# Performance work log

Hardware: AMD Instinct MI355X
Metric: run time of the kernel (lower is better)

The kernel has to match this reference:

```python
import jax, jax.numpy as jnp
import numpy as np

N_NODES = 100000
N_EDGES = 1600000
IN_F = 256
OUT_F = 128


def setup_inputs() -> dict:
    key = jax.random.key(0)
    ks = jax.random.split(key, 6)
    stdv = 1.0 / np.sqrt(OUT_F)
    x = jax.random.normal(ks[0], (N_NODES, IN_F), dtype=jnp.float32)
    edge_row = jax.random.randint(ks[1], (N_EDGES,), 0, N_NODES)
    edge_col = jax.random.randint(ks[2], (N_EDGES,), 0, N_NODES)
    edge_val = jax.random.uniform(ks[3], (N_EDGES,), dtype=jnp.float32)
    weight = jax.random.uniform(ks[4], (IN_F, OUT_F), minval=-stdv, maxval=stdv, dtype=jnp.float32)
    bias = jax.random.uniform(ks[5], (OUT_F,), minval=-stdv, maxval=stdv, dtype=jnp.float32)
    return {"x": x, "edge_row": edge_row, "edge_col": edge_col,
            "edge_val": edge_val, "weight": weight, "bias": bias}


def reference(x, edge_row, edge_col, edge_val, weight, bias):
    # support = input @ W                       [N, out]
    support = x @ weight
    # output = spmm(adj, support): for each edge (r, c, v),
    # out[r] += v * support[c]  -- gather then segment-sum over destinations.
    gathered = support[edge_col] * edge_val[:, None]   # [E, out]
    out = jax.ops.segment_sum(gathered, edge_row, num_segments=N_NODES)
    return out + bias
```

## Files before the change

### kernel.cpp

```cpp
#include <hip/hip_runtime.h>
#include <hip/hip_bf16.h>

#define N_NODES 100000
#define N_EDGES 1600000
#define IN_F 256
#define OUT_F 128

#define NBUCK 782
#define CH 4096
#define NCHB ((N_EDGES + CH - 1) / CH)
#define HCAP 2048
#define BCAP 3072

typedef __attribute__((ext_vector_type(8))) short bhalf8;
typedef __attribute__((ext_vector_type(4))) float f32x4;

static __device__ __forceinline__ unsigned short f2bfs(float f) {
    __hip_bfloat16 h = __float2bfloat16(f);
    return *reinterpret_cast<unsigned short*>(&h);
}

__global__ __launch_bounds__(256) void wt_kernel(
    const float* __restrict__ W, unsigned short* __restrict__ Wt)
{
    const int idx = blockIdx.x * 256 + threadIdx.x;
    const int col = idx >> 8;
    const int k   = idx & 255;
    Wt[idx] = f2bfs(W[(size_t)k * OUT_F + col]);
}

__global__ __launch_bounds__(512) void gemm_mfma_kernel(
    const float* __restrict__ x, const unsigned short* __restrict__ Wt,
    unsigned short* __restrict__ support)
{
    __shared__ unsigned short Bs[128 * 256];

    const int tid = threadIdx.x;

    {
        const int row = tid >> 2;
        const int q   = tid & 3;
        const uint4* src = (const uint4*)(Wt + (size_t)row * 256);
        uint4* dst       = (uint4*)(Bs + (size_t)row * 256);
        const int sw = row & 7;
        #pragma unroll
        for (int i = q * 8; i < q * 8 + 8; ++i)
            dst[i ^ sw] = src[i];
    }
    __syncthreads();

    const int wave = tid >> 6, lane = tid & 63;
    const int r_lo = lane & 15;
    const int kq   = lane >> 4;
    const int row0 = blockIdx.x * 128 + wave * 16;

    const float* xa = x + (size_t)min(row0 + r_lo, N_NODES - 1) * IN_F + kq * 8;

    f32x4 acc[8];
    #pragma unroll
    for (int c = 0; c < 8; ++c) acc[c] = (f32x4)0.f;

    #pragma unroll
    for (int ks = 0; ks < 8; ++ks) {
        const float4 al = *(const float4*)(xa + ks * 32);
        const float4 ah = *(const float4*)(xa + ks * 32 + 4);

        bhalf8 A;
        A[0] = (short)f2bfs(al.x); A[1] = (short)f2bfs(al.y);
        A[2] = (short)f2bfs(al.z); A[3] = (short)f2bfs(al.w);
        A[4] = (short)f2bfs(ah.x); A[5] = (short)f2bfs(ah.y);
        A[6] = (short)f2bfs(ah.z); A[7] = (short)f2bfs(ah.w);

        #pragma unroll
        for (int cf = 0; cf < 8; ++cf) {
            const int col = cf * 16 + r_lo;
            const int off = ((ks * 32 + kq * 8) ^ ((col & 7) << 3));
            const bhalf8 B = *(const bhalf8*)(Bs + (size_t)col * 256 + off);
            acc[cf] = __builtin_amdgcn_mfma_f32_16x16x32_bf16(A, B, acc[cf], 0, 0, 0);
        }
    }

    #pragma unroll
    for (int r = 0; r < 4; ++r) {
        const int row = row0 + kq * 4 + r;
        if (row < N_NODES) {
            unsigned short* dst = support + (size_t)row * OUT_F + r_lo;
            #pragma unroll
            for (int cf = 0; cf < 8; ++cf)
                dst[cf * 16] = f2bfs(acc[cf][r]);
        }
    }
}

__global__ __launch_bounds__(512) void bscatter_kernel(
    const int* __restrict__ erow, const int* __restrict__ ecol,
    const float* __restrict__ eval, int* __restrict__ bcnt,
    int2* __restrict__ ebuf)
{
    __shared__ int h[NBUCK];
    __shared__ int cur[NBUCK];
    __shared__ int gbase[NBUCK];
    __shared__ int ps[512];
    __shared__ unsigned short bb[CH];
    __shared__ int2 buf[CH];

    const int tid = threadIdx.x;
    const int e0  = blockIdx.x * CH;
    const int e1  = min(e0 + CH, N_EDGES);
    const int n   = e1 - e0;

    for (int i = tid; i < NBUCK; i += 512) h[i] = 0;
    __syncthreads();

    for (int e = e0 + tid; e < e1; e += 512)
        atomicAdd(&h[erow[e] >> 7], 1);
    __syncthreads();

    {
        const int idx0 = tid * 2;
        int sum = 0;
        #pragma unroll
        for (int k = 0; k < 2; ++k) { const int ii = idx0 + k; if (ii < NBUCK) sum += h[ii]; }
        ps[tid] = sum;
        __syncthreads();
        for (int off = 1; off < 512; off <<= 1) {
            const int a  = (tid >= off) ? ps[tid - off] : 0;
            const int x0 = ps[tid];
            __syncthreads();
            ps[tid] = x0 + a;
            __syncthreads();
        }
        int run = (tid == 0) ? 0 : ps[tid - 1];
        #pragma unroll
        for (int k = 0; k < 2; ++k) {
            const int ii = idx0 + k;
            if (ii < NBUCK) { cur[ii] = run; run += h[ii]; }
        }
    }
    __syncthreads();

    for (int e = e0 + tid; e < e1; e += 512) {
        const int r = erow[e];
        const int b = r >> 7;
        const int p = atomicAdd(&cur[b], 1);
        buf[p] = make_int2(((r & 127) << 17) | ecol[e], __float_as_int(eval[e]));
        bb[p]  = (unsigned short)b;
    }
    __syncthreads();

    for (int i = tid; i < NBUCK; i += 512)
        gbase[i] = h[i] ? (i * BCAP + atomicAdd(&bcnt[i], h[i])) : 0;
    __syncthreads();

    for (int i = tid; i < n; i += 512) {
        const int b  = bb[i];
        const int lb = cur[b] - h[b];
        ebuf[gbase[b] + (i - lb)] = buf[i];
    }
}

__global__ __launch_bounds__(256) void hspmm_kernel(
    const int* __restrict__ bcnt, const int2* __restrict__ ebuf,
    const unsigned short* __restrict__ support,
    const float* __restrict__ bias, float* __restrict__ out)
{
    __shared__ int2 srt[HCAP];
    __shared__ int rc[64];
    __shared__ int rb[65];
    __shared__ int cc[64];

    const int blk = blockIdx.x;
    const int pb  = blk >> 1;
    const unsigned hf = blk & 1;
    const int row0 = (pb << 7) + ((int)hf << 6);
    if (row0 >= N_NODES) return;
    const int nrows = min(64, N_NODES - row0);

    const int tid  = threadIdx.x;
    const int wave = tid >> 6, lane = tid & 63;
    const int lg   = lane >> 4;
    const int l4   = lane & 15;

    const int beg = pb * BCAP;
    const int end = beg + bcnt[pb];

    if (tid < 64) rc[tid] = 0;
    __syncthreads();

    for (int i = beg + tid; i < end; i += 256) {
        const unsigned ex = (unsigned)ebuf[i].x;
        const unsigned lr7 = (ex >> 17) & 127u;
        if ((lr7 >> 6) == hf) atomicAdd(&rc[lr7 & 63], 1);
    }
    __syncthreads();

    if (tid < 64) {
        int v = rc[tid];
        #pragma unroll
        for (int off = 1; off < 64; off <<= 1) {
            const int t = __shfl_up(v, off);
            if (lane >= off) v += t;
        }
        rb[tid + 1] = v;
        cc[tid] = v - rc[tid];
        if (tid == 0) rb[0] = 0;
    }
    __syncthreads();

    for (int i = beg + tid; i < end; i += 256) {
        const int2 e = ebuf[i];
        const unsigned lr7 = ((unsigned)e.x >> 17) & 127u;
        if ((lr7 >> 6) == hf)
            srt[atomicAdd(&cc[lr7 & 63], 1)] = e;
    }
    __syncthreads();

#define ACC(V, U)                                            \
    a0 += (V) * __uint_as_float((U).x << 16);                \
    a1 += (V) * __uint_as_float((U).x & 0xFFFF0000u);        \
    a2 += (V) * __uint_as_float((U).y << 16);                \
    a3 += (V) * __uint_as_float((U).y & 0xFFFF0000u);        \
    a4 += (V) * __uint_as_float((U).z << 16);                \
    a5 += (V) * __uint_as_float((U).z & 0xFFFF0000u);        \
    a6 += (V) * __uint_as_float((U).w << 16);                \
    a7 += (V) * __uint_as_float((U).w & 0xFFFF0000u);

    const float4 bv0 = *(const float4*)(bias + l4 * 8);
    const float4 bv1 = *(const float4*)(bias + l4 * 8 + 4);

    for (int lr = wave; lr < nrows; lr += 4) {
        const int s  = rb[lr];
        const int t2 = rb[lr + 1];
        float a0 = 0.f, a1 = 0.f, a2 = 0.f, a3 = 0.f;
        float a4 = 0.f, a5 = 0.f, a6 = 0.f, a7 = 0.f;
        int j = s;
        for (; j + 16 <= t2; j += 16) {
            const int2 e0 = srt[j      + lg];
            const int2 e1 = srt[j + 4  + lg];
            const int2 e2 = srt[j + 8  + lg];
            const int2 e3 = srt[j + 12 + lg];
            const uint4 u0 = *(const uint4*)(support + ((size_t)(e0.x & 0x1FFFF) << 7) + l4 * 8);
            const uint4 u1 = *(const uint4*)(support + ((size_t)(e1.x & 0x1FFFF) << 7) + l4 * 8);
            const uint4 u2 = *(const uint4*)(support + ((size_t)(e2.x & 0x1FFFF) << 7) + l4 * 8);
            const uint4 u3 = *(const uint4*)(support + ((size_t)(e3.x & 0x1FFFF) << 7) + l4 * 8);
            const float v0 = __int_as_float(e0.y), v1 = __int_as_float(e1.y);
            const float v2 = __int_as_float(e2.y), v3 = __int_as_float(e3.y);
            ACC(v0, u0) ACC(v1, u1) ACC(v2, u2) ACC(v3, u3)
        }
        for (; j + 4 <= t2; j += 4) {
            const int2 e = srt[j + lg];
            const uint4 u = *(const uint4*)(support + ((size_t)(e.x & 0x1FFFF) << 7) + l4 * 8);
            const float v = __int_as_float(e.y);
            ACC(v, u)
        }
        if (j < t2) {
            const int jj = min(j + lg, t2 - 1);
            const int2 e = srt[jj];
            const uint4 u = *(const uint4*)(support + ((size_t)(e.x & 0x1FFFF) << 7) + l4 * 8);
            const float v = (j + lg < t2) ? __int_as_float(e.y) : 0.f;
            ACC(v, u)
        }
        a0 += __shfl_xor(a0, 16); a0 += __shfl_xor(a0, 32);
        a1 += __shfl_xor(a1, 16); a1 += __shfl_xor(a1, 32);
        a2 += __shfl_xor(a2, 16); a2 += __shfl_xor(a2, 32);
        a3 += __shfl_xor(a3, 16); a3 += __shfl_xor(a3, 32);
        a4 += __shfl_xor(a4, 16); a4 += __shfl_xor(a4, 32);
        a5 += __shfl_xor(a5, 16); a5 += __shfl_xor(a5, 32);
        a6 += __shfl_xor(a6, 16); a6 += __shfl_xor(a6, 32);
        a7 += __shfl_xor(a7, 16); a7 += __shfl_xor(a7, 32);
        if (lane < 16) {
            float4* o = (float4*)(out + ((size_t)(row0 + lr) << 7) + l4 * 8);
            o[0] = make_float4(a0 + bv0.x, a1 + bv0.y, a2 + bv0.z, a3 + bv0.w);
            o[1] = make_float4(a4 + bv1.x, a5 + bv1.y, a6 + bv1.z, a7 + bv1.w);
        }
    }
#undef ACC
}

extern "C" void kernel_launch(void* const* d_in, const int* in_sizes, int n_in,
                              void* d_out, int out_size, void* d_ws, size_t ws_size,
                              hipStream_t stream) {
    const float* x    = (const float*)d_in[0];
    const int*   erow = (const int*)  d_in[1];
    const int*   ecol = (const int*)  d_in[2];
    const float* eval = (const float*)d_in[3];
    const float* W    = (const float*)d_in[4];
    const float* bias = (const float*)d_in[5];
    float*       out  = (float*)d_out;

    char* ws = (char*)d_ws;
    unsigned short* support = (unsigned short*)ws; ws += (size_t)N_NODES * OUT_F * 2;
    unsigned short* Wt      = (unsigned short*)ws; ws += (size_t)OUT_F * IN_F * 2;
    int*  bcnt  = (int*)ws;                        ws += 3136;
    int2* ebuf  = (int2*)ws;                       ws += (size_t)NBUCK * BCAP * 8;

    hipMemsetAsync(bcnt, 0, NBUCK * 4, stream);

    wt_kernel<<<(OUT_F * IN_F) / 256, 256, 0, stream>>>(W, Wt);
    gemm_mfma_kernel<<<(N_NODES + 127) / 128, 512, 0, stream>>>(x, Wt, support);

    bscatter_kernel<<<NCHB, 512, 0, stream>>>(erow, ecol, eval, bcnt, ebuf);

    hspmm_kernel<<<NBUCK * 2, 256, 0, stream>>>(bcnt, ebuf, support, bias, out);
}
```

Before: 133.4 us.

## Assign one 16-lane group per destination row in SpMM instead of one wave

The per-row SpMM mapping changes from one 64-lane wave per row, which split edges across four 16-lane subgroups and reduced with cross-lane shuffles, to one 16-lane group per row with 16 rows processed concurrently per block. This removes the shuffle reduction, the masked tail handling, and the idle lanes during the store. In exchange, each wave now covers four rows with different edge counts, so lanes can diverge when row degrees differ. Each group also walks its edges serially, which lowers memory-level parallelism per row.

```diff
diff --git a/kernel.cpp b/kernel.cpp
--- a/kernel.cpp
+++ b/kernel.cpp
@@ -177,9 +177,9 @@
     const int nrows = min(64, N_NODES - row0);
 
     const int tid  = threadIdx.x;
-    const int wave = tid >> 6, lane = tid & 63;
-    const int lg   = lane >> 4;
-    const int l4   = lane & 15;
+    const int lane = tid & 63;
+    const int grp  = tid >> 4;
+    const int l4   = tid & 15;
 
     const int beg = pb * BCAP;
     const int end = beg + bcnt[pb];
@@ -228,17 +228,15 @@
     const float4 bv0 = *(const float4*)(bias + l4 * 8);
     const float4 bv1 = *(const float4*)(bias + l4 * 8 + 4);
 
-    for (int lr = wave; lr < nrows; lr += 4) {
+    for (int lr = grp; lr < nrows; lr += 16) {
         const int s  = rb[lr];
         const int t2 = rb[lr + 1];
         float a0 = 0.f, a1 = 0.f, a2 = 0.f, a3 = 0.f;
         float a4 = 0.f, a5 = 0.f, a6 = 0.f, a7 = 0.f;
         int j = s;
-        for (; j + 16 <= t2; j += 16) {
-            const int2 e0 = srt[j      + lg];
-            const int2 e1 = srt[j + 4  + lg];
-            const int2 e2 = srt[j + 8  + lg];
-            const int2 e3 = srt[j + 12 + lg];
+        for (; j + 4 <= t2; j += 4) {
+            const int2 e0 = srt[j],     e1 = srt[j + 1];
+            const int2 e2 = srt[j + 2], e3 = srt[j + 3];
             const uint4 u0 = *(const uint4*)(support + ((size_t)(e0.x & 0x1FFFF) << 7) + l4 * 8);
             const uint4 u1 = *(const uint4*)(support + ((size_t)(e1.x & 0x1FFFF) << 7) + l4 * 8);
             const uint4 u2 = *(const uint4*)(support + ((size_t)(e2.x & 0x1FFFF) << 7) + l4 * 8);
@@ -247,32 +245,15 @@
             const float v2 = __int_as_float(e2.y), v3 = __int_as_float(e3.y);
             ACC(v0, u0) ACC(v1, u1) ACC(v2, u2) ACC(v3, u3)
         }
-        for (; j + 4 <= t2; j += 4) {
-            const int2 e = srt[j + lg];
+        for (; j < t2; ++j) {
+            const int2 e = srt[j];
             const uint4 u = *(const uint4*)(support + ((size_t)(e.x & 0x1FFFF) << 7) + l4 * 8);
             const float v = __int_as_float(e.y);
             ACC(v, u)
         }
-        if (j < t2) {
-            const int jj = min(j + lg, t2 - 1);
-            const int2 e = srt[jj];
-            const uint4 u = *(const uint4*)(support + ((size_t)(e.x & 0x1FFFF) << 7) + l4 * 8);
-            const float v = (j + lg < t2) ? __int_as_float(e.y) : 0.f;
-            ACC(v, u)
-        }
-        a0 += __shfl_xor(a0, 16); a0 += __shfl_xor(a0, 32);
-        a1 += __shfl_xor(a1, 16); a1 += __shfl_xor(a1, 32);
-        a2 += __shfl_xor(a2, 16); a2 += __shfl_xor(a2, 32);
-        a3 += __shfl_xor(a3, 16); a3 += __shfl_xor(a3, 32);
-        a4 += __shfl_xor(a4, 16); a4 += __shfl_xor(a4, 32);
-        a5 += __shfl_xor(a5, 16); a5 += __shfl_xor(a5, 32);
-        a6 += __shfl_xor(a6, 16); a6 += __shfl_xor(a6, 32);
-        a7 += __shfl_xor(a7, 16); a7 += __shfl_xor(a7, 32);
-        if (lane < 16) {
-            float4* o = (float4*)(out + ((size_t)(row0 + lr) << 7) + l4 * 8);
-            o[0] = make_float4(a0 + bv0.x, a1 + bv0.y, a2 + bv0.z, a3 + bv0.w);
-            o[1] = make_float4(a4 + bv1.x, a5 + bv1.y, a6 + bv1.z, a7 + bv1.w);
-        }
+        float4* o = (float4*)(out + ((size_t)(row0 + lr) << 7) + l4 * 8);
+        o[0] = make_float4(a0 + bv0.x, a1 + bv0.y, a2 + bv0.z, a3 + bv0.w);
+        o[1] = make_float4(a4 + bv1.x, a5 + bv1.y, a6 + bv1.z, a7 + bv1.w);
     }
 #undef ACC
 }
```

After: 132.1 us. Within noise of the previous version (-0.9%).
